# Performance work log

Measured on AMD Instinct MI355X. Metric: run time of the kernel, lower is better.

The kernel has to match this reference:

```python
import jax, jax.numpy as jnp
import numpy as np

FS = 3        # filter_size
STRIDE = 2
UPPER_PAD = 1
D_MODEL = 512


def setup_inputs() -> dict:
    key = jax.random.key(0)
    k1, k2, k3, k4 = jax.random.split(key, 4)
    b, h, n, d = 4, 8, 2048, D_MODEL
    nc = n // STRIDE
    layer_query = jax.random.normal(k1, (b, h, n, d), dtype=jnp.float32)
    uncompress_in = jax.random.normal(k2, (b, h, nc, d), dtype=jnp.float32)
    # nn.Linear(d*FS, d): weight (d, d*FS), bias (d,)
    W = jax.random.normal(k3, (d, d * FS), dtype=jnp.float32) * 0.02
    bias = jax.random.normal(k4, (d,), dtype=jnp.float32) * 0.01
    return {"layer_query": layer_query, "uncompress_in": uncompress_in,
            "W": W, "bias": bias, "i": 0}


def reference(layer_query, uncompress_in, W, bias, i):
    b, h, n, d = layer_query.shape
    # einsum('ijac,b->ijcab', u, kron_kernel) with kernel=[1,0,...] followed by
    # flatten(-2,-1) == transpose to (b,h,d,nc) then zero-upsample by STRIDE.
    u = jnp.swapaxes(uncompress_in, -1, -2)                      # (b,h,d,nc)
    nc = u.shape[-1]
    t = jnp.zeros(u.shape + (STRIDE,), u.dtype).at[..., 0].set(u)
    t = t.reshape(b, h, d, nc * STRIDE)                          # (b,h,d,nc*S)
    pad = FS - UPPER_PAD - 1
    t = jnp.pad(t, ((0, 0), (0, 0), (0, 0), (pad, pad)))
    # unfold(-1, FS, 1) then keep first n windows: window w covers t[..., w:w+FS]
    windows = jnp.stack([t[..., k:k + n] for k in range(FS)], axis=-1)  # (b,h,d,n,FS)
    up = jnp.transpose(windows, (0, 1, 3, 4, 2))                 # (b,h,n,FS,d)
    res_connect = up.sum(axis=3) / FS                            # (b,h,n,d)
    flat = up.reshape(b, h, n, FS * d)                           # (b,h,n,FS*d)
    out = jax.nn.relu(jnp.einsum('bhnk,dk->bhnd', flat, W) + bias)
    # dropout p=0.0 -> identity
    return layer_query + out + res_connect
```

## Files before the change

kernel.cpp:

```cpp
#include <hip/hip_runtime.h>
#include <cstdint>

#define NC    1024
#define D     512
#define KTOT  512
#define MTOT  32768
#define BK    64

typedef short  short8  __attribute__((ext_vector_type(8)));
typedef float  floatx4 __attribute__((ext_vector_type(4)));

__device__ inline void gl2lds16(const void* gptr, void* lptr) {
  __builtin_amdgcn_global_load_lds(
      (const __attribute__((address_space(1))) void*)gptr,
      (__attribute__((address_space(3))) void*)lptr,
      16, 0, 0);
}

__device__ inline unsigned short f2bf_rne(float f) {
  union { float f; unsigned u; } x; x.f = f;
  unsigned r = x.u + 0x7fffu + ((x.u >> 16) & 1u);
  return (unsigned short)(r >> 16);
}

__global__ __launch_bounds__(256) void cvt_f32_bf16(
    const float* __restrict__ src, unsigned short* __restrict__ dst, int n4) {
  int i = blockIdx.x * 256 + threadIdx.x;
  if (i >= n4) return;
  float4 v = ((const float4*)src)[i];
  ushort4 o;
  o.x = f2bf_rne(v.x); o.y = f2bf_rne(v.y);
  o.z = f2bf_rne(v.z); o.w = f2bf_rne(v.w);
  ((ushort4*)dst)[i] = o;
}

__global__ __launch_bounds__(256, 2) void fused_uncompress_gemm(
    const unsigned short* __restrict__ Ub,
    const unsigned short* __restrict__ Wb,
    const float* __restrict__ U32,
    const float* __restrict__ LQ,
    const float* __restrict__ bias,
    float* __restrict__ out)
{
  __shared__ __attribute__((aligned(16))) unsigned char smem[129*128 + 192*128];
  unsigned char* smemA = smem;
  unsigned char* smemB = smem + 129*128;

  const int tileM = blockIdx.x >> 3;
  const int tileN = blockIdx.x & 7;
  const int r0 = tileM * 128;
  const int n0 = tileN * 64;
  const int tid  = threadIdx.x;
  const int wv   = tid >> 6;
  const int ln   = tid & 63;
  const int quad = ln >> 4;
  const int am   = ln & 15;

  floatx4 acc[2][12];
  #pragma unroll
  for (int rt = 0; rt < 2; ++rt)
    #pragma unroll
    for (int ct = 0; ct < 12; ++ct)
      acc[rt][ct] = floatx4{0.f, 0.f, 0.f, 0.f};

  const bool zeroExtra = (((r0 + 128) & (NC - 1)) == 0);

  for (int kc = 0; kc < KTOT / BK; ++kc) {
    const int k0 = kc * BK;

    #pragma unroll
    for (int i = 0; i < 4; ++i) {
      int row = wv * 32 + i * 8 + (ln >> 3);
      int s   = ln & 7;
      int kch = s ^ (row & 7);
      const unsigned short* g = Ub + (size_t)(r0 + row) * KTOT + k0 + kch * 8;
      gl2lds16(g, smemA + (wv * 32 + i * 8) * 128);
    }
    if (wv == 0 && ln < 8) {
      if (zeroExtra) {
        *(float4*)(smemA + 128 * 128 + ln * 16) = make_float4(0.f, 0.f, 0.f, 0.f);
      } else {
        const unsigned short* g = Ub + (size_t)(r0 + 128) * KTOT + k0 + ln * 8;
        gl2lds16(g, smemA + 128 * 128);
      }
    }
    #pragma unroll
    for (int i = 0; i < 6; ++i) {
      int rho = wv * 48 + i * 8 + (ln >> 3);
      int s   = ln & 7;
      int kch = s ^ (rho & 7);
      int beta = rho >> 6;
      int nl   = rho & 63;
      const unsigned short* g =
          Wb + (size_t)(n0 + nl) * 1536 + beta * 512 + k0 + kch * 8;
      gl2lds16(g, smemB + (wv * 48 + i * 8) * 128);
    }
    __syncthreads();

    #pragma unroll
    for (int ks = 0; ks < 2; ++ks) {
      short8 a0[2], a1[2];
      #pragma unroll
      for (int rt = 0; rt < 2; ++rt) {
        int row  = wv * 32 + rt * 16 + am;
        int sl   = (ks * 4 + quad) ^ (row & 7);
        a0[rt] = *(const short8*)(smemA + row * 128 + sl * 16);
        int row1 = row + 1;
        int sl1  = (ks * 4 + quad) ^ (row1 & 7);
        a1[rt] = *(const short8*)(smemA + row1 * 128 + sl1 * 16);
      }
      #pragma unroll
      for (int ct = 0; ct < 12; ++ct) {
        int beta = ct >> 2;
        int nl   = (ct & 3) * 16 + am;
        int rho  = beta * 64 + nl;
        int sl   = (ks * 4 + quad) ^ (nl & 7);
        short8 b = *(const short8*)(smemB + rho * 128 + sl * 16);
        #pragma unroll
        for (int rt = 0; rt < 2; ++rt) {
          acc[rt][ct] = __builtin_amdgcn_mfma_f32_16x16x32_bf16(
              (beta == 2) ? a1[rt] : a0[rt], b, acc[rt][ct], 0, 0, 0);
        }
      }
    }
    __syncthreads();
  }

  const float inv3 = 1.0f / 3.0f;
  #pragma unroll
  for (int dt = 0; dt < 4; ++dt) {
    int col = n0 + dt * 16 + am;
    float bv = bias[col];
    #pragma unroll
    for (int rt = 0; rt < 2; ++rt) {
      #pragma unroll
      for (int r = 0; r < 4; ++r) {
        int jl = wv * 32 + rt * 16 + quad * 4 + r;
        int j  = r0 + jl;
        int head = j >> 10;
        int jn   = j & (NC - 1);
        size_t ob = ((size_t)head * 2048 + 2 * jn) * D + col;
        float p0 = acc[rt][dt][r];
        float p1 = acc[rt][4 + dt][r];
        float p2 = acc[rt][8 + dt][r];
        float uj  = U32[(size_t)j * D + col];
        float uj1 = (jn == NC - 1) ? 0.f : U32[(size_t)(j + 1) * D + col];
        float e = fmaxf(p1 + bv, 0.f);
        float o = fmaxf(p0 + p2 + bv, 0.f);
        out[ob]     = LQ[ob]     + e + uj * inv3;
        out[ob + D] = LQ[ob + D] + o + (uj + uj1) * inv3;
      }
    }
  }
}

extern "C" void kernel_launch(void* const* d_in, const int* in_sizes, int n_in,
                              void* d_out, int out_size, void* d_ws, size_t ws_size,
                              hipStream_t stream) {
  const float* LQ   = (const float*)d_in[0];
  const float* U32  = (const float*)d_in[1];
  const float* W    = (const float*)d_in[2];
  const float* bias = (const float*)d_in[3];
  float* out = (float*)d_out;

  unsigned short* Ub = (unsigned short*)d_ws;
  unsigned short* Wb = (unsigned short*)((char*)d_ws + (size_t)MTOT * KTOT * 2);

  const int n4U = MTOT * KTOT / 4;
  const int n4W = 512 * 1536 / 4;
  cvt_f32_bf16<<<(n4U + 255) / 256, 256, 0, stream>>>(U32, Ub, n4U);
  cvt_f32_bf16<<<(n4W + 255) / 256, 256, 0, stream>>>(W, Wb, n4W);

  fused_uncompress_gemm<<<dim3(2048), dim3(256), 0, stream>>>(
      Ub, Wb, U32, LQ, bias, out);
}
```

Baseline: 374.6 us.

## Drop LDS staging and load MFMA operands directly from global memory

The GEMM kernel stops staging A and B tiles in shared memory and has each wave load its MFMA fragments straight from global memory through L1/L2. Waves are rearranged into a 2x2 grid with 4 row tiles by 6 column tiles each, the K loop is fully unrolled, and the occupancy hint is raised to 3 blocks. This removes the LDS traffic and the barriers. The residual term now reads the bf16 copy of U instead of fp32, which halves that traffic but lowers the residual's precision. Each fragment is now reloaded redundantly by several waves, and the uncoalesced 16-byte global reads may become the bottleneck.

New measurement: 556.8 us. +48.6%, slower.

```diff
diff --git a/kernel.cpp b/kernel.cpp
--- a/kernel.cpp
+++ b/kernel.cpp
@@ -5,22 +5,18 @@
 #define D     512
 #define KTOT  512
 #define MTOT  32768
-#define BK    64
 
 typedef short  short8  __attribute__((ext_vector_type(8)));
 typedef float  floatx4 __attribute__((ext_vector_type(4)));
-
-__device__ inline void gl2lds16(const void* gptr, void* lptr) {
-  __builtin_amdgcn_global_load_lds(
-      (const __attribute__((address_space(1))) void*)gptr,
-      (__attribute__((address_space(3))) void*)lptr,
-      16, 0, 0);
-}
 
 __device__ inline unsigned short f2bf_rne(float f) {
   union { float f; unsigned u; } x; x.f = f;
   unsigned r = x.u + 0x7fffu + ((x.u >> 16) & 1u);
   return (unsigned short)(r >> 16);
+}
+
+__device__ inline float bf2f(unsigned short u) {
+  union { unsigned u; float f; } x; x.u = ((unsigned)u) << 16; return x.f;
 }
 
 __global__ __launch_bounds__(256) void cvt_f32_bf16(
@@ -34,18 +30,13 @@
   ((ushort4*)dst)[i] = o;
 }
 
-__global__ __launch_bounds__(256, 2) void fused_uncompress_gemm(
+__global__ __launch_bounds__(256, 3) void fused_uncompress_gemm(
     const unsigned short* __restrict__ Ub,
     const unsigned short* __restrict__ Wb,
-    const float* __restrict__ U32,
     const float* __restrict__ LQ,
     const float* __restrict__ bias,
     float* __restrict__ out)
 {
-  __shared__ __attribute__((aligned(16))) unsigned char smem[129*128 + 192*128];
-  unsigned char* smemA = smem;
-  unsigned char* smemB = smem + 129*128;
-
   const int tileM = blockIdx.x >> 3;
   const int tileN = blockIdx.x & 7;
   const int r0 = tileM * 128;
@@ -53,98 +44,79 @@
   const int tid  = threadIdx.x;
   const int wv   = tid >> 6;
   const int ln   = tid & 63;
+  const int wr   = wv >> 1;
+  const int wc   = wv & 1;
   const int quad = ln >> 4;
   const int am   = ln & 15;
 
-  floatx4 acc[2][12];
+  const short8* aPtr[4];
+  bool zeroA1[4];
   #pragma unroll
-  for (int rt = 0; rt < 2; ++rt)
+  for (int rt = 0; rt < 4; ++rt) {
+    int row = r0 + wr * 64 + rt * 16 + am;
+    aPtr[rt] = (const short8*)(Ub + (size_t)row * KTOT + quad * 8);
+    zeroA1[rt] = (((row + 1) & (NC - 1)) == 0);
+  }
+  const short8* bPtr[2];
+  #pragma unroll
+  for (int c = 0; c < 2; ++c) {
+    int brow = n0 + wc * 32 + c * 16 + am;
+    bPtr[c] = (const short8*)(Wb + (size_t)brow * 1536 + quad * 8);
+  }
+
+  floatx4 acc[4][6];
+  #pragma unroll
+  for (int rt = 0; rt < 4; ++rt)
     #pragma unroll
-    for (int ct = 0; ct < 12; ++ct)
+    for (int ct = 0; ct < 6; ++ct)
       acc[rt][ct] = floatx4{0.f, 0.f, 0.f, 0.f};
 
-  const bool zeroExtra = (((r0 + 128) & (NC - 1)) == 0);
-
-  for (int kc = 0; kc < KTOT / BK; ++kc) {
-    const int k0 = kc * BK;
-
+  #pragma unroll
+  for (int kc = 0; kc < 16; ++kc) {
+    const int ko = kc * 4;
+    short8 a0[4], a1[4];
     #pragma unroll
-    for (int i = 0; i < 4; ++i) {
-      int row = wv * 32 + i * 8 + (ln >> 3);
-      int s   = ln & 7;
-      int kch = s ^ (row & 7);
-      const unsigned short* g = Ub + (size_t)(r0 + row) * KTOT + k0 + kch * 8;
-      gl2lds16(g, smemA + (wv * 32 + i * 8) * 128);
+    for (int rt = 0; rt < 4; ++rt) {
+      a0[rt] = aPtr[rt][ko];
+      short8 t = aPtr[rt][ko + 64];
+      if (zeroA1[rt]) t = (short8)0;
+      a1[rt] = t;
     }
-    if (wv == 0 && ln < 8) {
-      if (zeroExtra) {
-        *(float4*)(smemA + 128 * 128 + ln * 16) = make_float4(0.f, 0.f, 0.f, 0.f);
-      } else {
-        const unsigned short* g = Ub + (size_t)(r0 + 128) * KTOT + k0 + ln * 8;
-        gl2lds16(g, smemA + 128 * 128);
+    short8 b[6];
+    #pragma unroll
+    for (int ct = 0; ct < 6; ++ct) {
+      int beta = ct >> 1, c = ct & 1;
+      b[ct] = bPtr[c][ko + beta * 64];
+    }
+    #pragma unroll
+    for (int ct = 0; ct < 6; ++ct) {
+      int beta = ct >> 1;
+      #pragma unroll
+      for (int rt = 0; rt < 4; ++rt) {
+        acc[rt][ct] = __builtin_amdgcn_mfma_f32_16x16x32_bf16(
+            (beta == 2) ? a1[rt] : a0[rt], b[ct], acc[rt][ct], 0, 0, 0);
       }
     }
-    #pragma unroll
-    for (int i = 0; i < 6; ++i) {
-      int rho = wv * 48 + i * 8 + (ln >> 3);
-      int s   = ln & 7;
-      int kch = s ^ (rho & 7);
-      int beta = rho >> 6;
-      int nl   = rho & 63;
-      const unsigned short* g =
-          Wb + (size_t)(n0 + nl) * 1536 + beta * 512 + k0 + kch * 8;
-      gl2lds16(g, smemB + (wv * 48 + i * 8) * 128);
-    }
-    __syncthreads();
-
-    #pragma unroll
-    for (int ks = 0; ks < 2; ++ks) {
-      short8 a0[2], a1[2];
-      #pragma unroll
-      for (int rt = 0; rt < 2; ++rt) {
-        int row  = wv * 32 + rt * 16 + am;
-        int sl   = (ks * 4 + quad) ^ (row & 7);
-        a0[rt] = *(const short8*)(smemA + row * 128 + sl * 16);
-        int row1 = row + 1;
-        int sl1  = (ks * 4 + quad) ^ (row1 & 7);
-        a1[rt] = *(const short8*)(smemA + row1 * 128 + sl1 * 16);
-      }
-      #pragma unroll
-      for (int ct = 0; ct < 12; ++ct) {
-        int beta = ct >> 2;
-        int nl   = (ct & 3) * 16 + am;
-        int rho  = beta * 64 + nl;
-        int sl   = (ks * 4 + quad) ^ (nl & 7);
-        short8 b = *(const short8*)(smemB + rho * 128 + sl * 16);
-        #pragma unroll
-        for (int rt = 0; rt < 2; ++rt) {
-          acc[rt][ct] = __builtin_amdgcn_mfma_f32_16x16x32_bf16(
-              (beta == 2) ? a1[rt] : a0[rt], b, acc[rt][ct], 0, 0, 0);
-        }
-      }
-    }
-    __syncthreads();
   }
 
   const float inv3 = 1.0f / 3.0f;
   #pragma unroll
-  for (int dt = 0; dt < 4; ++dt) {
-    int col = n0 + dt * 16 + am;
+  for (int csub = 0; csub < 2; ++csub) {
+    int col = n0 + wc * 32 + csub * 16 + am;
     float bv = bias[col];
     #pragma unroll
-    for (int rt = 0; rt < 2; ++rt) {
+    for (int rt = 0; rt < 4; ++rt) {
       #pragma unroll
       for (int r = 0; r < 4; ++r) {
-        int jl = wv * 32 + rt * 16 + quad * 4 + r;
-        int j  = r0 + jl;
+        int j  = r0 + wr * 64 + rt * 16 + quad * 4 + r;
         int head = j >> 10;
         int jn   = j & (NC - 1);
         size_t ob = ((size_t)head * 2048 + 2 * jn) * D + col;
-        float p0 = acc[rt][dt][r];
-        float p1 = acc[rt][4 + dt][r];
-        float p2 = acc[rt][8 + dt][r];
-        float uj  = U32[(size_t)j * D + col];
-        float uj1 = (jn == NC - 1) ? 0.f : U32[(size_t)(j + 1) * D + col];
+        float p0 = acc[rt][0 + csub][r];
+        float p1 = acc[rt][2 + csub][r];
+        float p2 = acc[rt][4 + csub][r];
+        float uj  = bf2f(Ub[(size_t)j * D + col]);
+        float uj1 = (jn == NC - 1) ? 0.f : bf2f(Ub[(size_t)(j + 1) * D + col]);
         float e = fmaxf(p1 + bv, 0.f);
         float o = fmaxf(p0 + p2 + bv, 0.f);
         out[ob]     = LQ[ob]     + e + uj * inv3;
@@ -172,5 +144,5 @@
   cvt_f32_bf16<<<(n4W + 255) / 256, 256, 0, stream>>>(W, Wb, n4W);
 
   fused_uncompress_gemm<<<dim3(2048), dim3(256), 0, stream>>>(
-      Ub, Wb, U32, LQ, bias, out);
+      Ub, Wb, LQ, bias, out);
 }
```
